# Performance work log

Hardware: AMD Instinct MI355X
Metric: run time of the kernel (lower is better)

Reference implementation:

```python
import jax, jax.numpy as jnp
import numpy as np

N0, N1, N2 = 200000, 50000, 10000   # source nodes, hop-1 targets, final targets
D, C, DEG = 256, 40, 10


def _sage(x_src, x_tgt, row, col, n_tgt, Wl, Wr, b, reduce):
    # PyG SAGEConv: lin_l(aggr(messages)) + lin_r(x_target); bias on lin_l only
    msg = x_src[row]                                   # [E, D] gather
    if reduce == 'mean':
        s = jax.ops.segment_sum(msg, col, num_segments=n_tgt)
        cnt = jax.ops.segment_sum(jnp.ones((row.shape[0], 1), msg.dtype), col, num_segments=n_tgt)
        agg = s / jnp.maximum(cnt, 1.0)
    else:
        agg = jax.ops.segment_max(msg, col, num_segments=n_tgt)
    return agg @ Wl + b + x_tgt @ Wr


def setup_inputs() -> dict:
    key = jax.random.key(0)
    ks = jax.random.split(key, 16)
    x = jax.random.normal(ks[0], (N0, D), jnp.float32)
    # every target gets exactly DEG sampled neighbors (NeighborSampler-style)
    row0 = jax.random.randint(ks[1], (N1 * DEG,), 0, N0, jnp.int32)
    col0 = jnp.repeat(jnp.arange(N1, dtype=jnp.int32), DEG)
    edge_index0 = jnp.stack([row0, col0])
    row1 = jax.random.randint(ks[2], (N2 * DEG,), 0, N1, jnp.int32)
    col1 = jnp.repeat(jnp.arange(N2, dtype=jnp.int32), DEG)
    edge_index1 = jnp.stack([row1, col1])
    s = 1.0 / np.sqrt(D)
    w = lambda k, shp: jax.random.uniform(k, shp, jnp.float32, -s, s)
    return {
        'x': x, 'edge_index0': edge_index0, 'edge_index1': edge_index1,
        'Wl_m0': w(ks[3], (D, D)), 'Wr_m0': w(ks[4], (D, D)), 'b_m0': jnp.zeros((D,), jnp.float32),
        'Wl_x0': w(ks[5], (D, D)), 'Wr_x0': w(ks[6], (D, D)), 'b_x0': jnp.zeros((D,), jnp.float32),
        'Wl_m1': w(ks[7], (D, D)), 'Wr_m1': w(ks[8], (D, D)), 'b_m1': jnp.zeros((D,), jnp.float32),
        'Wl_x1': w(ks[9], (D, D)), 'Wr_x1': w(ks[10], (D, D)), 'b_x1': jnp.zeros((D,), jnp.float32),
        'W_post': w(ks[11], (2 * D, C)), 'b_post': jnp.zeros((C,), jnp.float32),
    }


def reference(x, edge_index0, edge_index1,
              Wl_m0, Wr_m0, b_m0, Wl_x0, Wr_x0, b_x0,
              Wl_m1, Wr_m1, b_m1, Wl_x1, Wr_x1, b_x1,
              W_post, b_post):
    row0, col0 = edge_index0[0], edge_index0[1]
    row1, col1 = edge_index1[0], edge_index1[1]
    tgt0 = x[:N1]
    h_m = jax.nn.relu(_sage(x, tgt0, row0, col0, N1, Wl_m0, Wr_m0, b_m0, 'mean'))
    h_x = jax.nn.relu(_sage(x, tgt0, row0, col0, N1, Wl_x0, Wr_x0, b_x0, 'max'))
    # NOTE: faithful to source bug: layer-1 target features are the RAW x[:size[1]]
    tgt1 = x[:N2]
    o_m = _sage(h_m, tgt1, row1, col1, N2, Wl_m1, Wr_m1, b_m1, 'mean')
    o_x = _sage(h_x, tgt1, row1, col1, N2, Wl_x1, Wr_x1, b_x1, 'max')
    out = jnp.concatenate([o_m, o_x], axis=-1) @ W_post + b_post
    return jax.nn.log_softmax(out, axis=-1)
```

## Files before the change

kernel.cpp:

```cpp
#include <hip/hip_runtime.h>
#include <hip/hip_bf16.h>
#include <math.h>

#define N0v 200000
#define N1v 50000
#define N2v 10000
#define Dv  256
#define Cv  40
#define DEGv 10

typedef __attribute__((ext_vector_type(8))) short          s16x8;
typedef __attribute__((ext_vector_type(8))) unsigned short u16x8;
typedef __attribute__((ext_vector_type(4))) float          f32x4;

static __device__ __forceinline__ unsigned short f2bf(float f) {
    __hip_bfloat16 h = __float2bfloat16(f);
    return *reinterpret_cast<unsigned short*>(&h);
}
static __device__ __forceinline__ float bf2f(unsigned short u) {
    __hip_bfloat16 h = *reinterpret_cast<__hip_bfloat16*>(&u);
    return __bfloat162float(h);
}

static __device__ __forceinline__ void gload16(const void* g, void* l) {
    __builtin_amdgcn_global_load_lds(
        (const __attribute__((address_space(1))) unsigned int*)g,
        (__attribute__((address_space(3))) unsigned int*)l, 16, 0, 0);
}

__global__ __launch_bounds__(256) void agg0_prep_kernel(
    const float* __restrict__ x, const int* __restrict__ row,
    unsigned short* __restrict__ om, unsigned short* __restrict__ ox,
    unsigned short* __restrict__ xtb,
    const float* __restrict__ Wl0, const float* __restrict__ Wr0,
    const float* __restrict__ Wl1, const float* __restrict__ Wr1,
    const float* __restrict__ Wl2, const float* __restrict__ Wr2,
    const float* __restrict__ Wl3, const float* __restrict__ Wr3,
    unsigned short* __restrict__ WT0, unsigned short* __restrict__ WT1,
    unsigned short* __restrict__ WT2, unsigned short* __restrict__ WT3)
{
    const int b = blockIdx.x;
    if (b < 12500) {
        const int t = b * 4 + (threadIdx.x >> 6);
        const int c = threadIdx.x & 63;
        const int eb = t * DEGv;
        float4 s = make_float4(0.f, 0.f, 0.f, 0.f);
        float4 mx = make_float4(-INFINITY, -INFINITY, -INFINITY, -INFINITY);
#pragma unroll
        for (int k = 0; k < DEGv; ++k) {
            const int r = row[eb + k];
            float4 v = ((const float4*)x)[(size_t)r * 64 + c];
            s.x += v.x; s.y += v.y; s.z += v.z; s.w += v.w;
            mx.x = fmaxf(mx.x, v.x); mx.y = fmaxf(mx.y, v.y);
            mx.z = fmaxf(mx.z, v.z); mx.w = fmaxf(mx.w, v.w);
        }
        const float inv = 1.0f / DEGv;
        unsigned short osum[4] = { f2bf(s.x * inv), f2bf(s.y * inv), f2bf(s.z * inv), f2bf(s.w * inv) };
        unsigned short omax[4] = { f2bf(mx.x), f2bf(mx.y), f2bf(mx.z), f2bf(mx.w) };
        *(uint2*)&om[(size_t)t * Dv + c * 4] = *(uint2*)osum;
        *(uint2*)&ox[(size_t)t * Dv + c * 4] = *(uint2*)omax;

        float4 v = ((const float4*)x)[(size_t)t * 64 + c];
        unsigned short o[4] = { f2bf(v.x), f2bf(v.y), f2bf(v.z), f2bf(v.w) };
        *(uint2*)&xtb[(size_t)t * Dv + c * 4] = *(uint2*)o;
    } else {
        const int idx = b - 12500;
        const int p = idx >> 8;
        const int n = idx & 255;
        const int k = threadIdx.x;
        const float* Wl = (p == 0) ? Wl0 : (p == 1) ? Wl1 : (p == 2) ? Wl2 : Wl3;
        const float* Wr = (p == 0) ? Wr0 : (p == 1) ? Wr1 : (p == 2) ? Wr2 : Wr3;
        unsigned short* WT = (p == 0) ? WT0 : (p == 1) ? WT1 : (p == 2) ? WT2 : WT3;
        WT[(size_t)n * 512 + k]       = f2bf(Wl[(size_t)k * Dv + n]);
        WT[(size_t)n * 512 + 256 + k] = f2bf(Wr[(size_t)k * Dv + n]);
    }
}

__global__ __launch_bounds__(256) void agg1_kernel(
    const unsigned short* __restrict__ hm, const unsigned short* __restrict__ hx,
    const int* __restrict__ row,
    unsigned short* __restrict__ om, unsigned short* __restrict__ ox)
{
    const int t = blockIdx.x * 8 + (threadIdx.x >> 5);
    const int c = threadIdx.x & 31;
    const int eb = t * DEGv;
    float s[8] = {};
    float mx[8] = { -INFINITY, -INFINITY, -INFINITY, -INFINITY,
                    -INFINITY, -INFINITY, -INFINITY, -INFINITY };
#pragma unroll
    for (int k = 0; k < DEGv; ++k) {
        const int r = row[eb + k];
        u16x8 vm = ((const u16x8*)hm)[(size_t)r * 32 + c];
        u16x8 vx = ((const u16x8*)hx)[(size_t)r * 32 + c];
#pragma unroll
        for (int j = 0; j < 8; ++j) {
            s[j]  += bf2f(vm[j]);
            mx[j]  = fmaxf(mx[j], bf2f(vx[j]));
        }
    }
    const float inv = 1.0f / DEGv;
    unsigned short osum[8], omax[8];
#pragma unroll
    for (int j = 0; j < 8; ++j) { osum[j] = f2bf(s[j] * inv); omax[j] = f2bf(mx[j]); }
    *(u16x8*)&om[(size_t)t * Dv + c * 8] = *(u16x8*)osum;
    *(u16x8*)&ox[(size_t)t * Dv + c * 8] = *(u16x8*)omax;
}

template<int RELU, int OUTBF>
__global__ __launch_bounds__(256) void gemm_mfma_kernel(
    const unsigned short* __restrict__ A1a, const unsigned short* __restrict__ A1b,
    const unsigned short* __restrict__ A2,
    const unsigned short* __restrict__ WTa, const unsigned short* __restrict__ WTb,
    const float* __restrict__ biasa, const float* __restrict__ biasb,
    void* outa, void* outb, int M, int ldc, int col_step)
{
    __shared__ unsigned short Asb[128 * 64];
    __shared__ unsigned short Bsb[256 * 64];

    const int z = blockIdx.z;
    const unsigned short* A1 = z ? A1b : A1a;
    const unsigned short* WT = z ? WTb : WTa;
    const float* bias = z ? biasb : biasa;
    void* outp = z ? outb : outa;
    const int col_off = z * col_step;

    const int tid  = threadIdx.x;
    const int lane = tid & 63;
    const int w    = tid >> 6;
    const int wrow = w >> 1;
    const int wcol = w & 1;
    const int m0   = blockIdx.x * 128;

    const int lrow = lane >> 3;
    const int scol = ((lane & 7) ^ lrow) * 8;

    const unsigned short* pA1[4];
    const unsigned short* pA2[4];
    unsigned short* lA[4];
#pragma unroll
    for (int c = 0; c < 4; ++c) {
        const int r = w * 32 + c * 8 + lrow;
        int gm = m0 + r; if (gm >= M) gm = M - 1;
        pA1[c] = A1 + (size_t)gm * Dv + scol;
        pA2[c] = A2 + (size_t)gm * Dv + scol;
        lA[c] = &Asb[(w * 32 + c * 8) * 64];
    }
    const unsigned short* pB[8];
    unsigned short* lB[8];
#pragma unroll
    for (int c = 0; c < 8; ++c) {
        const int r = w * 64 + c * 8 + lrow;
        pB[c] = WT + (size_t)r * 512 + scol;
        lB[c] = &Bsb[(w * 64 + c * 8) * 64];
    }

    const int fr = lane & 15;
    const int f7 = lane & 7;

    f32x4 acc[4][8] = {};

    for (int k0 = 0; k0 < 512; k0 += 64) {
        __syncthreads();
        if (k0 < 256) {
#pragma unroll
            for (int c = 0; c < 4; ++c) gload16(pA1[c] + k0, lA[c]);
        } else {
#pragma unroll
            for (int c = 0; c < 4; ++c) gload16(pA2[c] + (k0 - 256), lA[c]);
        }
#pragma unroll
        for (int c = 0; c < 8; ++c) gload16(pB[c] + k0, lB[c]);
        __syncthreads();

#pragma unroll
        for (int kk = 0; kk < 2; ++kk) {
            const int sl = kk * 4 + (lane >> 4);
            const int so = ((sl ^ f7) << 3);
            s16x8 af[4];
#pragma unroll
            for (int i = 0; i < 4; ++i)
                af[i] = *(const s16x8*)&Asb[(wrow * 64 + i * 16 + fr) * 64 + so];
#pragma unroll
            for (int j = 0; j < 8; ++j) {
                s16x8 bv = *(const s16x8*)&Bsb[(wcol * 128 + j * 16 + fr) * 64 + so];
#pragma unroll
                for (int i = 0; i < 4; ++i)
                    acc[i][j] = __builtin_amdgcn_mfma_f32_16x16x32_bf16(af[i], bv, acc[i][j], 0, 0, 0);
            }
        }
    }

#pragma unroll
    for (int i = 0; i < 4; ++i) {
#pragma unroll
        for (int reg = 0; reg < 4; ++reg) {
            const int gr = m0 + wrow * 64 + i * 16 + (lane >> 4) * 4 + reg;
            if (gr < M) {
#pragma unroll
                for (int j = 0; j < 8; ++j) {
                    const int gc = wcol * 128 + j * 16 + fr;
                    float v = acc[i][j][reg] + bias[gc];
                    if (RELU) v = fmaxf(v, 0.0f);
                    if (OUTBF)
                        ((unsigned short*)outp)[(size_t)gr * ldc + col_off + gc] = f2bf(v);
                    else
                        ((float*)outp)[(size_t)gr * ldc + col_off + gc] = v;
                }
            }
        }
    }
}

__global__ __launch_bounds__(256) void post_kernel(
    const unsigned short* __restrict__ ocat, const float* __restrict__ Wp,
    const float* __restrict__ bp, float* __restrict__ out, int nrows)
{
    __shared__ float sW[512 * 40];
    __shared__ float sP[7][32][40];
    __shared__ float sb[Cv];

    const int tid = threadIdx.x;

    for (int i = tid; i < 5120; i += 256)
        ((float4*)sW)[i] = ((const float4*)Wp)[i];
    if (tid < Cv) sb[tid] = bp[tid];
    __syncthreads();

    const int q = tid >> 5;
    const int r = tid & 31;
    const int t = blockIdx.x * 32 + r;
    const bool valid = (t < nrows);

    float acc[Cv] = {};
    if (valid) {
        const unsigned short* prow = ocat + (size_t)t * 512 + q * 64;
        for (int kk = 0; kk < 64; kk += 8) {
            u16x8 v = *(const u16x8*)(prow + kk);
            const float* wbase = &sW[(q * 64 + kk) * Cv];
#pragma unroll
            for (int e = 0; e < 8; ++e) {
                const float xv = bf2f(v[e]);
                const float* wr_ = wbase + e * Cv;
#pragma unroll
                for (int c4 = 0; c4 < Cv; c4 += 4) {
                    f32x4 wv = *(const f32x4*)(wr_ + c4);
                    acc[c4 + 0] += xv * wv[0];
                    acc[c4 + 1] += xv * wv[1];
                    acc[c4 + 2] += xv * wv[2];
                    acc[c4 + 3] += xv * wv[3];
                }
            }
        }
    }

    if (q > 0) {
#pragma unroll
        for (int c4 = 0; c4 < Cv; c4 += 4)
            *(f32x4*)&sP[q - 1][r][c4] = *(f32x4*)&acc[c4];
    }
    __syncthreads();

    if (q == 0 && valid) {
#pragma unroll
        for (int p = 0; p < 7; ++p)
#pragma unroll
            for (int c4 = 0; c4 < Cv; c4 += 4) {
                f32x4 pv = *(const f32x4*)&sP[p][r][c4];
                acc[c4 + 0] += pv[0];
                acc[c4 + 1] += pv[1];
                acc[c4 + 2] += pv[2];
                acc[c4 + 3] += pv[3];
            }
        float m = -INFINITY;
#pragma unroll
        for (int c = 0; c < Cv; ++c) { acc[c] += sb[c]; m = fmaxf(m, acc[c]); }
        float s = 0.0f;
#pragma unroll
        for (int c = 0; c < Cv; ++c) s += expf(acc[c] - m);
        const float lse = m + logf(s);
        float* dst = out + (size_t)t * Cv;
#pragma unroll
        for (int c4 = 0; c4 < Cv; c4 += 4) {
            float o[4] = { acc[c4] - lse, acc[c4 + 1] - lse, acc[c4 + 2] - lse, acc[c4 + 3] - lse };
            *(float4*)(dst + c4) = *(float4*)o;
        }
    }
}

extern "C" void kernel_launch(void* const* d_in, const int* in_sizes, int n_in,
                              void* d_out, int out_size, void* d_ws, size_t ws_size,
                              hipStream_t stream)
{
    const float* x      = (const float*)d_in[0];
    const int*   ei0    = (const int*)d_in[1];
    const int*   ei1    = (const int*)d_in[2];
    const float* Wl_m0  = (const float*)d_in[3];
    const float* Wr_m0  = (const float*)d_in[4];
    const float* b_m0   = (const float*)d_in[5];
    const float* Wl_x0  = (const float*)d_in[6];
    const float* Wr_x0  = (const float*)d_in[7];
    const float* b_x0   = (const float*)d_in[8];
    const float* Wl_m1  = (const float*)d_in[9];
    const float* Wr_m1  = (const float*)d_in[10];
    const float* b_m1   = (const float*)d_in[11];
    const float* Wl_x1  = (const float*)d_in[12];
    const float* Wr_x1  = (const float*)d_in[13];
    const float* b_x1   = (const float*)d_in[14];
    const float* W_post = (const float*)d_in[15];
    const float* b_post = (const float*)d_in[16];
    float* out = (float*)d_out;

    const int* row0 = ei0;
    const int* row1 = ei1;

    char* ws = (char*)d_ws;
    const size_t NB = (size_t)N1v * Dv * 2;
    unsigned short* xtb = (unsigned short*)(ws);
    unsigned short* am  = (unsigned short*)(ws + NB);
    unsigned short* ax  = (unsigned short*)(ws + 2 * NB);
    unsigned short* hm  = (unsigned short*)(ws + 3 * NB);
    unsigned short* hx  = (unsigned short*)(ws + 4 * NB);
    unsigned short* a1m = (unsigned short*)(ws + 5 * NB);
    unsigned short* a1x = a1m + (size_t)N2v * Dv;
    unsigned short* ocat = (unsigned short*)(ws + 5 * NB + (size_t)2 * N2v * Dv * 2);
    unsigned short* WT0m = ocat + (size_t)N2v * 2 * Dv;
    unsigned short* WT0x = WT0m + (size_t)256 * 512;
    unsigned short* WT1m = WT0x + (size_t)256 * 512;
    unsigned short* WT1x = WT1m + (size_t)256 * 512;

    const dim3 blk(256);

    agg0_prep_kernel<<<12500 + 1024, blk, 0, stream>>>(
        x, row0, am, ax, xtb,
        Wl_m0, Wr_m0, Wl_x0, Wr_x0, Wl_m1, Wr_m1, Wl_x1, Wr_x1,
        WT0m, WT0x, WT1m, WT1x);

    gemm_mfma_kernel<1, 1><<<dim3((N1v + 127) / 128, 1, 2), blk, 0, stream>>>(
        am, ax, xtb, WT0m, WT0x, b_m0, b_x0, hm, hx, N1v, Dv, 0);

    agg1_kernel<<<N2v / 8, blk, 0, stream>>>(hm, hx, row1, a1m, a1x);
    gemm_mfma_kernel<0, 1><<<dim3((N2v + 127) / 128, 1, 2), blk, 0, stream>>>(
        a1m, a1x, xtb, WT1m, WT1x, b_m1, b_x1, ocat, ocat, N2v, 2 * Dv, Dv);

    post_kernel<<<(N2v + 31) / 32, blk, 0, stream>>>(ocat, W_post, b_post, out, N2v);
}
```

Before: 217.7 us.

## Fuse neighbor aggregation into SAGE GEMM kernel with double-buffered weight staging

Replaces the separate aggregation kernels and GEMM kernels with one fused kernel per layer. Each 64-row block gathers its neighbors, computes mean and max into LDS as bf16, then runs MFMA against double-buffered transposed weights. The x-target half is read straight from fp32 x and converted in registers, so the xtb, am/ax and a1m/a1x intermediates and their HBM round trips go away. The cost is smaller tiles, 512-thread blocks, and the weight tiles being reloaded by every block. The per-tile global fp32 loads of x in the second half may also stall the MFMA loop.

New measurement: 303.7 us. +39.5%, slower.

```diff
diff --git a/kernel.cpp b/kernel.cpp
--- a/kernel.cpp
+++ b/kernel.cpp
@@ -28,10 +28,7 @@
         (__attribute__((address_space(3))) unsigned int*)l, 16, 0, 0);
 }
 
-__global__ __launch_bounds__(256) void agg0_prep_kernel(
-    const float* __restrict__ x, const int* __restrict__ row,
-    unsigned short* __restrict__ om, unsigned short* __restrict__ ox,
-    unsigned short* __restrict__ xtb,
+__global__ __launch_bounds__(256) void prep_kernel(
     const float* __restrict__ Wl0, const float* __restrict__ Wr0,
     const float* __restrict__ Wl1, const float* __restrict__ Wr1,
     const float* __restrict__ Wl2, const float* __restrict__ Wr2,
@@ -39,176 +36,170 @@
     unsigned short* __restrict__ WT0, unsigned short* __restrict__ WT1,
     unsigned short* __restrict__ WT2, unsigned short* __restrict__ WT3)
 {
-    const int b = blockIdx.x;
-    if (b < 12500) {
-        const int t = b * 4 + (threadIdx.x >> 6);
-        const int c = threadIdx.x & 63;
-        const int eb = t * DEGv;
-        float4 s = make_float4(0.f, 0.f, 0.f, 0.f);
-        float4 mx = make_float4(-INFINITY, -INFINITY, -INFINITY, -INFINITY);
-#pragma unroll
-        for (int k = 0; k < DEGv; ++k) {
-            const int r = row[eb + k];
-            float4 v = ((const float4*)x)[(size_t)r * 64 + c];
-            s.x += v.x; s.y += v.y; s.z += v.z; s.w += v.w;
-            mx.x = fmaxf(mx.x, v.x); mx.y = fmaxf(mx.y, v.y);
-            mx.z = fmaxf(mx.z, v.z); mx.w = fmaxf(mx.w, v.w);
-        }
-        const float inv = 1.0f / DEGv;
-        unsigned short osum[4] = { f2bf(s.x * inv), f2bf(s.y * inv), f2bf(s.z * inv), f2bf(s.w * inv) };
-        unsigned short omax[4] = { f2bf(mx.x), f2bf(mx.y), f2bf(mx.z), f2bf(mx.w) };
-        *(uint2*)&om[(size_t)t * Dv + c * 4] = *(uint2*)osum;
-        *(uint2*)&ox[(size_t)t * Dv + c * 4] = *(uint2*)omax;
-
-        float4 v = ((const float4*)x)[(size_t)t * 64 + c];
-        unsigned short o[4] = { f2bf(v.x), f2bf(v.y), f2bf(v.z), f2bf(v.w) };
-        *(uint2*)&xtb[(size_t)t * Dv + c * 4] = *(uint2*)o;
-    } else {
-        const int idx = b - 12500;
-        const int p = idx >> 8;
-        const int n = idx & 255;
-        const int k = threadIdx.x;
-        const float* Wl = (p == 0) ? Wl0 : (p == 1) ? Wl1 : (p == 2) ? Wl2 : Wl3;
-        const float* Wr = (p == 0) ? Wr0 : (p == 1) ? Wr1 : (p == 2) ? Wr2 : Wr3;
-        unsigned short* WT = (p == 0) ? WT0 : (p == 1) ? WT1 : (p == 2) ? WT2 : WT3;
-        WT[(size_t)n * 512 + k]       = f2bf(Wl[(size_t)k * Dv + n]);
-        WT[(size_t)n * 512 + 256 + k] = f2bf(Wr[(size_t)k * Dv + n]);
-    }
-}
-
-__global__ __launch_bounds__(256) void agg1_kernel(
-    const unsigned short* __restrict__ hm, const unsigned short* __restrict__ hx,
-    const int* __restrict__ row,
-    unsigned short* __restrict__ om, unsigned short* __restrict__ ox)
+    const int idx = blockIdx.x;
+    const int p = idx >> 8;
+    const int n = idx & 255;
+    const int k = threadIdx.x;
+    const float* Wl = (p == 0) ? Wl0 : (p == 1) ? Wl1 : (p == 2) ? Wl2 : Wl3;
+    const float* Wr = (p == 0) ? Wr0 : (p == 1) ? Wr1 : (p == 2) ? Wr2 : Wr3;
+    unsigned short* WT = (p == 0) ? WT0 : (p == 1) ? WT1 : (p == 2) ? WT2 : WT3;
+    WT[(size_t)n * 512 + k]       = f2bf(Wl[(size_t)k * Dv + n]);
+    WT[(size_t)n * 512 + 256 + k] = f2bf(Wr[(size_t)k * Dv + n]);
+}
+
+template<int L0T, int RELU>
+__global__ __launch_bounds__(512, 2) void fused_sage_kernel(
+    const float* __restrict__ x,
+    const unsigned short* __restrict__ gm, const unsigned short* __restrict__ gx,
+    const int* __restrict__ rowarr,
+    const unsigned short* __restrict__ WTm, const unsigned short* __restrict__ WTx,
+    const float* __restrict__ bm, const float* __restrict__ bx,
+    unsigned short* __restrict__ outm, unsigned short* __restrict__ outx,
+    int M, int ldc)
 {
-    const int t = blockIdx.x * 8 + (threadIdx.x >> 5);
-    const int c = threadIdx.x & 31;
-    const int eb = t * DEGv;
-    float s[8] = {};
-    float mx[8] = { -INFINITY, -INFINITY, -INFINITY, -INFINITY,
-                    -INFINITY, -INFINITY, -INFINITY, -INFINITY };
-#pragma unroll
-    for (int k = 0; k < DEGv; ++k) {
-        const int r = row[eb + k];
-        u16x8 vm = ((const u16x8*)hm)[(size_t)r * 32 + c];
-        u16x8 vx = ((const u16x8*)hx)[(size_t)r * 32 + c];
-#pragma unroll
-        for (int j = 0; j < 8; ++j) {
-            s[j]  += bf2f(vm[j]);
-            mx[j]  = fmaxf(mx[j], bf2f(vx[j]));
-        }
-    }
-    const float inv = 1.0f / DEGv;
-    unsigned short osum[8], omax[8];
-#pragma unroll
-    for (int j = 0; j < 8; ++j) { osum[j] = f2bf(s[j] * inv); omax[j] = f2bf(mx[j]); }
-    *(u16x8*)&om[(size_t)t * Dv + c * 8] = *(u16x8*)osum;
-    *(u16x8*)&ox[(size_t)t * Dv + c * 8] = *(u16x8*)omax;
-}
-
-template<int RELU, int OUTBF>
-__global__ __launch_bounds__(256) void gemm_mfma_kernel(
-    const unsigned short* __restrict__ A1a, const unsigned short* __restrict__ A1b,
-    const unsigned short* __restrict__ A2,
-    const unsigned short* __restrict__ WTa, const unsigned short* __restrict__ WTb,
-    const float* __restrict__ biasa, const float* __restrict__ biasb,
-    void* outa, void* outb, int M, int ldc, int col_step)
-{
-    __shared__ unsigned short Asb[128 * 64];
-    __shared__ unsigned short Bsb[256 * 64];
-
-    const int z = blockIdx.z;
-    const unsigned short* A1 = z ? A1b : A1a;
-    const unsigned short* WT = z ? WTb : WTa;
-    const float* bias = z ? biasb : biasa;
-    void* outp = z ? outb : outa;
-    const int col_off = z * col_step;
+    __shared__ unsigned short Asb[2][64][256];
+    __shared__ unsigned short Bsb[2][2][256][32];
 
     const int tid  = threadIdx.x;
     const int lane = tid & 63;
     const int w    = tid >> 6;
-    const int wrow = w >> 1;
+    const int m0   = blockIdx.x * 64;
+
+#define STAGE_B(bufv, k0v)                                                        \
+    {                                                                             \
+        _Pragma("unroll")                                                         \
+        for (int g = 0; g < 4; ++g) {                                             \
+            const int id  = g * 512 + tid;                                        \
+            const int st  = id >> 10;                                             \
+            const int id2 = id & 1023;                                            \
+            const int n   = id2 >> 2;                                             \
+            const int sl  = id2 & 3;                                              \
+            const unsigned short* srcp = (st ? WTx : WTm) + (size_t)n * 512 +     \
+                                         (k0v) + ((sl ^ ((n >> 1) & 3)) << 3);    \
+            unsigned short* ldst = &Bsb[bufv][0][0][0] + (size_t)(g * 512 + w * 64) * 8; \
+            gload16(srcp, ldst);                                                  \
+        }                                                                         \
+    }
+
+    STAGE_B(0, 0);
+
+    {
+        const int t0 = m0 + w * 8;
+        const bool fast = (t0 + 7 <= M - 1);
+        int i0 = 0, i1 = 0;
+        if (fast) {
+            i0 = rowarr[t0 * DEGv + lane];
+            i1 = rowarr[t0 * DEGv + 64 + (lane & 15)];
+        }
+        for (int i = 0; i < 8; ++i) {
+            const int lr = w * 8 + i;
+            const int t  = min(m0 + lr, M - 1);
+            float s0 = 0.f, s1 = 0.f, s2 = 0.f, s3 = 0.f;
+            float x0 = -INFINITY, x1 = -INFINITY, x2 = -INFINITY, x3 = -INFINITY;
+#pragma unroll
+            for (int k = 0; k < DEGv; ++k) {
+                int r;
+                if (fast) {
+                    const int flat = i * DEGv + k;
+                    r = (flat < 64) ? __shfl(i0, flat) : __shfl(i1, flat - 64);
+                } else {
+                    r = rowarr[t * DEGv + k];
+                }
+                if (L0T) {
+                    const float4 v = ((const float4*)x)[(size_t)r * 64 + lane];
+                    s0 += v.x; s1 += v.y; s2 += v.z; s3 += v.w;
+                    x0 = fmaxf(x0, v.x); x1 = fmaxf(x1, v.y);
+                    x2 = fmaxf(x2, v.z); x3 = fmaxf(x3, v.w);
+                } else {
+                    const uint2 a = *(const uint2*)(gm + (size_t)r * Dv + lane * 4);
+                    const uint2 b = *(const uint2*)(gx + (size_t)r * Dv + lane * 4);
+                    s0 += bf2f((unsigned short)(a.x & 0xffff));
+                    s1 += bf2f((unsigned short)(a.x >> 16));
+                    s2 += bf2f((unsigned short)(a.y & 0xffff));
+                    s3 += bf2f((unsigned short)(a.y >> 16));
+                    x0 = fmaxf(x0, bf2f((unsigned short)(b.x & 0xffff)));
+                    x1 = fmaxf(x1, bf2f((unsigned short)(b.x >> 16)));
+                    x2 = fmaxf(x2, bf2f((unsigned short)(b.y & 0xffff)));
+                    x3 = fmaxf(x3, bf2f((unsigned short)(b.y >> 16)));
+                }
+            }
+            const float inv = 1.0f / DEGv;
+            unsigned short om4[4] = { f2bf(s0 * inv), f2bf(s1 * inv), f2bf(s2 * inv), f2bf(s3 * inv) };
+            unsigned short ox4[4] = { f2bf(x0), f2bf(x1), f2bf(x2), f2bf(x3) };
+            const int eoff = (((lane >> 1) ^ (lr & 7)) << 3) + ((lane & 1) << 2);
+            *(uint2*)(&Asb[0][lr][0] + eoff) = *(const uint2*)om4;
+            *(uint2*)(&Asb[1][lr][0] + eoff) = *(const uint2*)ox4;
+        }
+    }
+
+    __syncthreads();
+
+    const int set  = w >> 2;
+    const int wrow = (w >> 1) & 1;
     const int wcol = w & 1;
-    const int m0   = blockIdx.x * 128;
-
-    const int lrow = lane >> 3;
-    const int scol = ((lane & 7) ^ lrow) * 8;
-
-    const unsigned short* pA1[4];
-    const unsigned short* pA2[4];
-    unsigned short* lA[4];
-#pragma unroll
-    for (int c = 0; c < 4; ++c) {
-        const int r = w * 32 + c * 8 + lrow;
-        int gm = m0 + r; if (gm >= M) gm = M - 1;
-        pA1[c] = A1 + (size_t)gm * Dv + scol;
-        pA2[c] = A2 + (size_t)gm * Dv + scol;
-        lA[c] = &Asb[(w * 32 + c * 8) * 64];
-    }
-    const unsigned short* pB[8];
-    unsigned short* lB[8];
-#pragma unroll
-    for (int c = 0; c < 8; ++c) {
-        const int r = w * 64 + c * 8 + lrow;
-        pB[c] = WT + (size_t)r * 512 + scol;
-        lB[c] = &Bsb[(w * 64 + c * 8) * 64];
-    }
-
-    const int fr = lane & 15;
-    const int f7 = lane & 7;
-
-    f32x4 acc[4][8] = {};
-
-    for (int k0 = 0; k0 < 512; k0 += 64) {
+    const int q    = lane >> 4;
+    const int fr   = lane & 15;
+
+    f32x4 acc[2][8] = {};
+
+    int cur = 0;
+    for (int step = 0; step < 16; ++step) {
+        const int k0 = step * 32;
+        if (step < 15) STAGE_B(cur ^ 1, k0 + 32);
+
+        s16x8 af[2];
+        if (k0 < 256) {
+#pragma unroll
+            for (int i = 0; i < 2; ++i) {
+                const int r = wrow * 32 + i * 16 + fr;
+                const int slot = ((k0 >> 3) + q) ^ (r & 7);
+                af[i] = *(const s16x8*)(&Asb[set][r][0] + (slot << 3));
+            }
+        } else {
+#pragma unroll
+            for (int i = 0; i < 2; ++i) {
+                const int t = min(m0 + wrow * 32 + i * 16 + fr, M - 1);
+                const float* p = x + (size_t)t * Dv + (k0 - 256) + q * 8;
+                const float4 u0 = *(const float4*)p;
+                const float4 u1 = *(const float4*)(p + 4);
+                unsigned short e[8] = { f2bf(u0.x), f2bf(u0.y), f2bf(u0.z), f2bf(u0.w),
+                                        f2bf(u1.x), f2bf(u1.y), f2bf(u1.z), f2bf(u1.w) };
+                af[i] = *(const s16x8*)e;
+            }
+        }
+
+#pragma unroll
+        for (int j = 0; j < 8; ++j) {
+            const int n = wcol * 128 + j * 16 + fr;
+            const int slotb = q ^ ((n >> 1) & 3);
+            const s16x8 bv = *(const s16x8*)(&Bsb[cur][set][n][0] + (slotb << 3));
+#pragma unroll
+            for (int i = 0; i < 2; ++i)
+                acc[i][j] = __builtin_amdgcn_mfma_f32_16x16x32_bf16(af[i], bv, acc[i][j], 0, 0, 0);
+        }
         __syncthreads();
-        if (k0 < 256) {
-#pragma unroll
-            for (int c = 0; c < 4; ++c) gload16(pA1[c] + k0, lA[c]);
-        } else {
-#pragma unroll
-            for (int c = 0; c < 4; ++c) gload16(pA2[c] + (k0 - 256), lA[c]);
-        }
-#pragma unroll
-        for (int c = 0; c < 8; ++c) gload16(pB[c] + k0, lB[c]);
-        __syncthreads();
-
-#pragma unroll
-        for (int kk = 0; kk < 2; ++kk) {
-            const int sl = kk * 4 + (lane >> 4);
-            const int so = ((sl ^ f7) << 3);
-            s16x8 af[4];
-#pragma unroll
-            for (int i = 0; i < 4; ++i)
-                af[i] = *(const s16x8*)&Asb[(wrow * 64 + i * 16 + fr) * 64 + so];
-#pragma unroll
-            for (int j = 0; j < 8; ++j) {
-                s16x8 bv = *(const s16x8*)&Bsb[(wcol * 128 + j * 16 + fr) * 64 + so];
-#pragma unroll
-                for (int i = 0; i < 4; ++i)
-                    acc[i][j] = __builtin_amdgcn_mfma_f32_16x16x32_bf16(af[i], bv, acc[i][j], 0, 0, 0);
-            }
-        }
-    }
-
-#pragma unroll
-    for (int i = 0; i < 4; ++i) {
+        cur ^= 1;
+    }
+
+    const float* bias = set ? bx : bm;
+    unsigned short* dst = set ? outx : outm;
+#pragma unroll
+    for (int i = 0; i < 2; ++i) {
 #pragma unroll
         for (int reg = 0; reg < 4; ++reg) {
-            const int gr = m0 + wrow * 64 + i * 16 + (lane >> 4) * 4 + reg;
+            const int gr = m0 + wrow * 32 + i * 16 + q * 4 + reg;
             if (gr < M) {
 #pragma unroll
                 for (int j = 0; j < 8; ++j) {
                     const int gc = wcol * 128 + j * 16 + fr;
                     float v = acc[i][j][reg] + bias[gc];
                     if (RELU) v = fmaxf(v, 0.0f);
-                    if (OUTBF)
-                        ((unsigned short*)outp)[(size_t)gr * ldc + col_off + gc] = f2bf(v);
-                    else
-                        ((float*)outp)[(size_t)gr * ldc + col_off + gc] = v;
+                    dst[(size_t)gr * ldc + gc] = f2bf(v);
                 }
             }
         }
     }
+#undef STAGE_B
 }
 
 __global__ __launch_bounds__(256) void post_kernel(
@@ -314,33 +305,23 @@
     const int* row1 = ei1;
 
     char* ws = (char*)d_ws;
-    const size_t NB = (size_t)N1v * Dv * 2;
-    unsigned short* xtb = (unsigned short*)(ws);
-    unsigned short* am  = (unsigned short*)(ws + NB);
-    unsigned short* ax  = (unsigned short*)(ws + 2 * NB);
-    unsigned short* hm  = (unsigned short*)(ws + 3 * NB);
-    unsigned short* hx  = (unsigned short*)(ws + 4 * NB);
-    unsigned short* a1m = (unsigned short*)(ws + 5 * NB);
-    unsigned short* a1x = a1m + (size_t)N2v * Dv;
-    unsigned short* ocat = (unsigned short*)(ws + 5 * NB + (size_t)2 * N2v * Dv * 2);
+    unsigned short* hm   = (unsigned short*)(ws);
+    unsigned short* hx   = hm + (size_t)N1v * Dv;
+    unsigned short* ocat = hx + (size_t)N1v * Dv;
     unsigned short* WT0m = ocat + (size_t)N2v * 2 * Dv;
     unsigned short* WT0x = WT0m + (size_t)256 * 512;
     unsigned short* WT1m = WT0x + (size_t)256 * 512;
     unsigned short* WT1x = WT1m + (size_t)256 * 512;
 
-    const dim3 blk(256);
-
-    agg0_prep_kernel<<<12500 + 1024, blk, 0, stream>>>(
-        x, row0, am, ax, xtb,
+    prep_kernel<<<1024, dim3(256), 0, stream>>>(
         Wl_m0, Wr_m0, Wl_x0, Wr_x0, Wl_m1, Wr_m1, Wl_x1, Wr_x1,
         WT0m, WT0x, WT1m, WT1x);
 
-    gemm_mfma_kernel<1, 1><<<dim3((N1v + 127) / 128, 1, 2), blk, 0, stream>>>(
-        am, ax, xtb, WT0m, WT0x, b_m0, b_x0, hm, hx, N1v, Dv, 0);
-
-    agg1_kernel<<<N2v / 8, blk, 0, stream>>>(hm, hx, row1, a1m, a1x);
-    gemm_mfma_kernel<0, 1><<<dim3((N2v + 127) / 128, 1, 2), blk, 0, stream>>>(
-        a1m, a1x, xtb, WT1m, WT1x, b_m1, b_x1, ocat, ocat, N2v, 2 * Dv, Dv);
-
-    post_kernel<<<(N2v + 31) / 32, blk, 0, stream>>>(ocat, W_post, b_post, out, N2v);
-}
+    fused_sage_kernel<1, 1><<<(N1v + 63) / 64, dim3(512), 0, stream>>>(
+        x, hm, hm, row0, WT0m, WT0x, b_m0, b_x0, hm, hx, N1v, Dv);
+
+    fused_sage_kernel<0, 0><<<(N2v + 63) / 64, dim3(512), 0, stream>>>(
+        x, hm, hx, row1, WT1m, WT1x, b_m1, b_x1, ocat, ocat + Dv, N2v, 2 * Dv);
+
+    post_kernel<<<(N2v + 31) / 32, dim3(256), 0, stream>>>(ocat, W_post, b_post, out, N2v);
+}
```

## Double-buffer GEMM LDS tiles with K=32 steps and a new swizzle

Applied to the files above, without the earlier changes.

Rewrites the MFMA GEMM main loop to use two LDS buffers with a K-step of 32. The next tile's global-to-LDS loads are issued before the current tile's MFMAs, so each iteration needs one barrier instead of two. The LDS layout changes to pack two rows per 64-element line with an XOR swizzle, and fragment offsets are precomputed. This aims to hide global load latency behind compute at the cost of more loop iterations and whatever the compiler does with waitcnt placement for the async loads.

After: 226.6 us. 1.04x slower.

```diff
diff --git a/kernel.cpp b/kernel.cpp
--- a/kernel.cpp
+++ b/kernel.cpp
@@ -114,8 +114,8 @@
     const float* __restrict__ biasa, const float* __restrict__ biasb,
     void* outa, void* outb, int M, int ldc, int col_step)
 {
-    __shared__ unsigned short Asb[128 * 64];
-    __shared__ unsigned short Bsb[256 * 64];
+    __shared__ unsigned short Asb[2][4096];
+    __shared__ unsigned short Bsb[2][8192];
 
     const int z = blockIdx.z;
     const unsigned short* A1 = z ? A1b : A1a;
@@ -126,75 +126,100 @@
 
     const int tid  = threadIdx.x;
     const int lane = tid & 63;
-    const int w    = tid >> 6;
-    const int wrow = w >> 1;
-    const int wcol = w & 1;
+    const int wrow = (tid >> 7) & 1;
+    const int wcol = (tid >> 6) & 1;
     const int m0   = blockIdx.x * 128;
 
-    const int lrow = lane >> 3;
-    const int scol = ((lane & 7) ^ lrow) * 8;
-
-    const unsigned short* pA1[4];
-    const unsigned short* pA2[4];
-    unsigned short* lA[4];
+    const unsigned short* pA1s[2];
+    const unsigned short* pA2s[2];
+    int ldsA[2];
+#pragma unroll
+    for (int c = 0; c < 2; ++c) {
+        const int p = tid + c * 256;
+        const int L = p >> 3, s = p & 7;
+        const int sig = s ^ (L & 7);
+        int gm = m0 + 2 * L + (sig >> 2);
+        if (gm >= M) gm = M - 1;
+        const int gk = (sig & 3) << 3;
+        pA1s[c] = A1 + (size_t)gm * Dv + gk;
+        pA2s[c] = A2 + (size_t)gm * Dv + gk;
+        ldsA[c] = p * 8;
+    }
+    const unsigned short* pBs[4];
+    int ldsB[4];
 #pragma unroll
     for (int c = 0; c < 4; ++c) {
-        const int r = w * 32 + c * 8 + lrow;
-        int gm = m0 + r; if (gm >= M) gm = M - 1;
-        pA1[c] = A1 + (size_t)gm * Dv + scol;
-        pA2[c] = A2 + (size_t)gm * Dv + scol;
-        lA[c] = &Asb[(w * 32 + c * 8) * 64];
-    }
-    const unsigned short* pB[8];
-    unsigned short* lB[8];
-#pragma unroll
-    for (int c = 0; c < 8; ++c) {
-        const int r = w * 64 + c * 8 + lrow;
-        pB[c] = WT + (size_t)r * 512 + scol;
-        lB[c] = &Bsb[(w * 64 + c * 8) * 64];
-    }
-
+        const int p = tid + c * 256;
+        const int L = p >> 3, s = p & 7;
+        const int sig = s ^ (L & 7);
+        const int n = 2 * L + (sig >> 2);
+        const int gk = (sig & 3) << 3;
+        pBs[c] = WT + (size_t)n * 512 + gk;
+        ldsB[c] = p * 8;
+    }
+
+#define STAGE(bufv, k0v)                                                     \
+    {                                                                        \
+        if ((k0v) < 256) {                                                   \
+            gload16(pA1s[0] + (k0v), &Asb[bufv][ldsA[0]]);                   \
+            gload16(pA1s[1] + (k0v), &Asb[bufv][ldsA[1]]);                   \
+        } else {                                                             \
+            gload16(pA2s[0] + ((k0v) - 256), &Asb[bufv][ldsA[0]]);           \
+            gload16(pA2s[1] + ((k0v) - 256), &Asb[bufv][ldsA[1]]);           \
+        }                                                                    \
+        _Pragma("unroll")                                                    \
+        for (int c = 0; c < 4; ++c)                                          \
+            gload16(pBs[c] + (k0v), &Bsb[bufv][ldsB[c]]);                    \
+    }
+
+    const int q  = lane >> 4;
     const int fr = lane & 15;
-    const int f7 = lane & 7;
+    int aoff[4];
+#pragma unroll
+    for (int i = 0; i < 4; ++i) {
+        const int r = wrow * 64 + i * 16 + fr;
+        const int L = r >> 1;
+        const int s = (((r & 1) << 2) + q) ^ (L & 7);
+        aoff[i] = L * 64 + s * 8;
+    }
+    int boff[8];
+#pragma unroll
+    for (int j = 0; j < 8; ++j) {
+        const int n = wcol * 128 + j * 16 + fr;
+        const int L = n >> 1;
+        const int s = (((n & 1) << 2) + q) ^ (L & 7);
+        boff[j] = L * 64 + s * 8;
+    }
 
     f32x4 acc[4][8] = {};
 
-    for (int k0 = 0; k0 < 512; k0 += 64) {
+    STAGE(0, 0);
+    __syncthreads();
+    int cur = 0;
+    for (int step = 0; step < 16; ++step) {
+        if (step < 15) STAGE(cur ^ 1, (step + 1) * 32);
+
+        s16x8 af[4];
+#pragma unroll
+        for (int i = 0; i < 4; ++i)
+            af[i] = *(const s16x8*)&Asb[cur][aoff[i]];
+#pragma unroll
+        for (int j = 0; j < 8; ++j) {
+            const s16x8 bv = *(const s16x8*)&Bsb[cur][boff[j]];
+#pragma unroll
+            for (int i = 0; i < 4; ++i)
+                acc[i][j] = __builtin_amdgcn_mfma_f32_16x16x32_bf16(af[i], bv, acc[i][j], 0, 0, 0);
+        }
         __syncthreads();
-        if (k0 < 256) {
-#pragma unroll
-            for (int c = 0; c < 4; ++c) gload16(pA1[c] + k0, lA[c]);
-        } else {
-#pragma unroll
-            for (int c = 0; c < 4; ++c) gload16(pA2[c] + (k0 - 256), lA[c]);
-        }
-#pragma unroll
-        for (int c = 0; c < 8; ++c) gload16(pB[c] + k0, lB[c]);
-        __syncthreads();
-
-#pragma unroll
-        for (int kk = 0; kk < 2; ++kk) {
-            const int sl = kk * 4 + (lane >> 4);
-            const int so = ((sl ^ f7) << 3);
-            s16x8 af[4];
-#pragma unroll
-            for (int i = 0; i < 4; ++i)
-                af[i] = *(const s16x8*)&Asb[(wrow * 64 + i * 16 + fr) * 64 + so];
-#pragma unroll
-            for (int j = 0; j < 8; ++j) {
-                s16x8 bv = *(const s16x8*)&Bsb[(wcol * 128 + j * 16 + fr) * 64 + so];
-#pragma unroll
-                for (int i = 0; i < 4; ++i)
-                    acc[i][j] = __builtin_amdgcn_mfma_f32_16x16x32_bf16(af[i], bv, acc[i][j], 0, 0, 0);
-            }
-        }
-    }
+        cur ^= 1;
+    }
+#undef STAGE
 
 #pragma unroll
     for (int i = 0; i < 4; ++i) {
 #pragma unroll
         for (int reg = 0; reg < 4; ++reg) {
-            const int gr = m0 + wrow * 64 + i * 16 + (lane >> 4) * 4 + reg;
+            const int gr = m0 + wrow * 64 + i * 16 + q * 4 + reg;
             if (gr < M) {
 #pragma unroll
                 for (int j = 0; j < 8; ++j) {
```

## Convert all of x to bf16 first, then gather bf16 rows in a separate agg0

Applied to the files above, without the earlier changes.

The fused first-hop aggregation that gathered fp32 rows of x is split in two. A prep kernel now converts the whole 200k-row x to bf16, and a new agg0 kernel gathers the half-size bf16 rows with 16-byte vector loads. The aim is to halve gather bytes and keep the bf16 copy resident in the large last-level cache. The cost is an extra full read of x, a write of the bf16 copy, one more kernel launch, and bf16 rounding of inputs before the mean and max.

After: 217.0 us. No clear change (-0.3%).

```diff
diff --git a/kernel.cpp b/kernel.cpp
--- a/kernel.cpp
+++ b/kernel.cpp
@@ -28,10 +28,8 @@
         (__attribute__((address_space(3))) unsigned int*)l, 16, 0, 0);
 }
 
-__global__ __launch_bounds__(256) void agg0_prep_kernel(
-    const float* __restrict__ x, const int* __restrict__ row,
-    unsigned short* __restrict__ om, unsigned short* __restrict__ ox,
-    unsigned short* __restrict__ xtb,
+__global__ __launch_bounds__(256) void conv_prep_kernel(
+    const float* __restrict__ x, unsigned short* __restrict__ xb,
     const float* __restrict__ Wl0, const float* __restrict__ Wr0,
     const float* __restrict__ Wl1, const float* __restrict__ Wr1,
     const float* __restrict__ Wl2, const float* __restrict__ Wr2,
@@ -40,40 +38,53 @@
     unsigned short* __restrict__ WT2, unsigned short* __restrict__ WT3)
 {
     const int b = blockIdx.x;
-    if (b < 12500) {
-        const int t = b * 4 + (threadIdx.x >> 6);
-        const int c = threadIdx.x & 63;
-        const int eb = t * DEGv;
-        float4 s = make_float4(0.f, 0.f, 0.f, 0.f);
-        float4 mx = make_float4(-INFINITY, -INFINITY, -INFINITY, -INFINITY);
-#pragma unroll
-        for (int k = 0; k < DEGv; ++k) {
-            const int r = row[eb + k];
-            float4 v = ((const float4*)x)[(size_t)r * 64 + c];
-            s.x += v.x; s.y += v.y; s.z += v.z; s.w += v.w;
-            mx.x = fmaxf(mx.x, v.x); mx.y = fmaxf(mx.y, v.y);
-            mx.z = fmaxf(mx.z, v.z); mx.w = fmaxf(mx.w, v.w);
-        }
-        const float inv = 1.0f / DEGv;
-        unsigned short osum[4] = { f2bf(s.x * inv), f2bf(s.y * inv), f2bf(s.z * inv), f2bf(s.w * inv) };
-        unsigned short omax[4] = { f2bf(mx.x), f2bf(mx.y), f2bf(mx.z), f2bf(mx.w) };
-        *(uint2*)&om[(size_t)t * Dv + c * 4] = *(uint2*)osum;
-        *(uint2*)&ox[(size_t)t * Dv + c * 4] = *(uint2*)omax;
-
-        float4 v = ((const float4*)x)[(size_t)t * 64 + c];
-        unsigned short o[4] = { f2bf(v.x), f2bf(v.y), f2bf(v.z), f2bf(v.w) };
-        *(uint2*)&xtb[(size_t)t * Dv + c * 4] = *(uint2*)o;
+    const int tid = threadIdx.x;
+    if (b < 25000) {
+        const size_t i = ((size_t)b * 256 + tid) * 8;
+        float4 v0 = *(const float4*)(x + i);
+        float4 v1 = *(const float4*)(x + i + 4);
+        unsigned short o[8] = { f2bf(v0.x), f2bf(v0.y), f2bf(v0.z), f2bf(v0.w),
+                                f2bf(v1.x), f2bf(v1.y), f2bf(v1.z), f2bf(v1.w) };
+        *(u16x8*)(xb + i) = *(u16x8*)o;
     } else {
-        const int idx = b - 12500;
+        const int idx = b - 25000;
         const int p = idx >> 8;
         const int n = idx & 255;
-        const int k = threadIdx.x;
         const float* Wl = (p == 0) ? Wl0 : (p == 1) ? Wl1 : (p == 2) ? Wl2 : Wl3;
         const float* Wr = (p == 0) ? Wr0 : (p == 1) ? Wr1 : (p == 2) ? Wr2 : Wr3;
         unsigned short* WT = (p == 0) ? WT0 : (p == 1) ? WT1 : (p == 2) ? WT2 : WT3;
-        WT[(size_t)n * 512 + k]       = f2bf(Wl[(size_t)k * Dv + n]);
-        WT[(size_t)n * 512 + 256 + k] = f2bf(Wr[(size_t)k * Dv + n]);
-    }
+        WT[(size_t)n * 512 + tid]       = f2bf(Wl[(size_t)tid * Dv + n]);
+        WT[(size_t)n * 512 + 256 + tid] = f2bf(Wr[(size_t)tid * Dv + n]);
+    }
+}
+
+__global__ __launch_bounds__(256) void agg0_kernel(
+    const unsigned short* __restrict__ xb, const int* __restrict__ row,
+    unsigned short* __restrict__ om, unsigned short* __restrict__ ox)
+{
+    const int t = blockIdx.x * 8 + (threadIdx.x >> 5);
+    const int c = threadIdx.x & 31;
+    const int eb = t * DEGv;
+    float s[8] = {};
+    float mx[8] = { -INFINITY, -INFINITY, -INFINITY, -INFINITY,
+                    -INFINITY, -INFINITY, -INFINITY, -INFINITY };
+#pragma unroll
+    for (int k = 0; k < DEGv; ++k) {
+        const int r = row[eb + k];
+        u16x8 v = ((const u16x8*)xb)[(size_t)r * 32 + c];
+#pragma unroll
+        for (int j = 0; j < 8; ++j) {
+            const float f = bf2f(v[j]);
+            s[j] += f;
+            mx[j] = fmaxf(mx[j], f);
+        }
+    }
+    const float inv = 1.0f / DEGv;
+    unsigned short osum[8], omax[8];
+#pragma unroll
+    for (int j = 0; j < 8; ++j) { osum[j] = f2bf(s[j] * inv); omax[j] = f2bf(mx[j]); }
+    *(u16x8*)&om[(size_t)t * Dv + c * 8] = *(u16x8*)osum;
+    *(u16x8*)&ox[(size_t)t * Dv + c * 8] = *(u16x8*)omax;
 }
 
 __global__ __launch_bounds__(256) void agg1_kernel(
@@ -314,15 +325,16 @@
     const int* row1 = ei1;
 
     char* ws = (char*)d_ws;
+    const size_t XB = (size_t)N0v * Dv * 2;
     const size_t NB = (size_t)N1v * Dv * 2;
-    unsigned short* xtb = (unsigned short*)(ws);
-    unsigned short* am  = (unsigned short*)(ws + NB);
-    unsigned short* ax  = (unsigned short*)(ws + 2 * NB);
-    unsigned short* hm  = (unsigned short*)(ws + 3 * NB);
-    unsigned short* hx  = (unsigned short*)(ws + 4 * NB);
-    unsigned short* a1m = (unsigned short*)(ws + 5 * NB);
+    unsigned short* xb  = (unsigned short*)(ws);
+    unsigned short* am  = (unsigned short*)(ws + XB);
+    unsigned short* ax  = (unsigned short*)(ws + XB + NB);
+    unsigned short* hm  = (unsigned short*)(ws + XB + 2 * NB);
+    unsigned short* hx  = (unsigned short*)(ws + XB + 3 * NB);
+    unsigned short* a1m = (unsigned short*)(ws + XB + 4 * NB);
     unsigned short* a1x = a1m + (size_t)N2v * Dv;
-    unsigned short* ocat = (unsigned short*)(ws + 5 * NB + (size_t)2 * N2v * Dv * 2);
+    unsigned short* ocat = (unsigned short*)(ws + XB + 4 * NB + (size_t)2 * N2v * Dv * 2);
     unsigned short* WT0m = ocat + (size_t)N2v * 2 * Dv;
     unsigned short* WT0x = WT0m + (size_t)256 * 512;
     unsigned short* WT1m = WT0x + (size_t)256 * 512;
@@ -330,17 +342,19 @@
 
     const dim3 blk(256);
 
-    agg0_prep_kernel<<<12500 + 1024, blk, 0, stream>>>(
-        x, row0, am, ax, xtb,
+    conv_prep_kernel<<<25000 + 1024, blk, 0, stream>>>(
+        x, xb,
         Wl_m0, Wr_m0, Wl_x0, Wr_x0, Wl_m1, Wr_m1, Wl_x1, Wr_x1,
         WT0m, WT0x, WT1m, WT1x);
 
+    agg0_kernel<<<N1v / 8, blk, 0, stream>>>(xb, row0, am, ax);
+
     gemm_mfma_kernel<1, 1><<<dim3((N1v + 127) / 128, 1, 2), blk, 0, stream>>>(
-        am, ax, xtb, WT0m, WT0x, b_m0, b_x0, hm, hx, N1v, Dv, 0);
+        am, ax, xb, WT0m, WT0x, b_m0, b_x0, hm, hx, N1v, Dv, 0);
 
     agg1_kernel<<<N2v / 8, blk, 0, stream>>>(hm, hx, row1, a1m, a1x);
     gemm_mfma_kernel<0, 1><<<dim3((N2v + 127) / 128, 1, 2), blk, 0, stream>>>(
-        a1m, a1x, xtb, WT1m, WT1x, b_m1, b_x1, ocat, ocat, N2v, 2 * Dv, Dv);
+        a1m, a1x, xb, WT1m, WT1x, b_m1, b_x1, ocat, ocat, N2v, 2 * Dv, Dv);
 
     post_kernel<<<(N2v + 31) / 32, blk, 0, stream>>>(ocat, W_post, b_post, out, N2v);
 }
```
